# Kernel tuning notes

Hardware: AMD Instinct MI355X
Metric: run time of the kernel (lower is better)

Reference implementation:

```python
import jax, jax.numpy as jnp
import numpy as np

B, T, C, NH = 4, 827, 1024, 16
HS = C // NH
SCALE = 1.0 / float(np.sqrt(HS))


def setup_inputs() -> dict:
    key = jax.random.key(0)
    ks = jax.random.split(key, 16)
    d = {}
    d["x"] = jax.random.normal(ks[0], (B, T, C), jnp.float32)
    d["x_kv"] = jax.random.normal(ks[1], (B, T, C), jnp.float32)
    d["h"] = jax.random.normal(ks[2], (B, NH, T, T), jnp.float32) * 0.1
    for i, name in enumerate(["f01", "f02", "f12", "b01", "b02", "b12"]):
        d[name] = jax.random.uniform(ks[3 + i], (B, 256, 256), jnp.float32)
    for i, name in enumerate(["Wq", "Wk", "Wv", "Wp"]):
        d[name] = jax.random.normal(ks[9 + i], (C, C), jnp.float32) * 0.02
    for name in ["bq", "bk", "bv", "bp"]:
        d[name] = jnp.zeros((C,), jnp.float32)
    return d


def _sm(a):
    return jax.nn.softmax(a, axis=-1)


def reference(x, x_kv, h, f01, f02, f12, b01, b02, b12,
              Wq, bq, Wk, bk, Wv, bv, Wp, bp):
    Bb, Tt, Cc = x.shape

    def heads(t):  # [B,T,C] -> [B,NH,T,HS]
        return t.reshape(Bb, Tt, NH, HS).transpose(0, 2, 1, 3)

    q = heads(x @ Wq.T + bq)
    k = heads(x_kv @ Wk.T + bk)
    v = heads(x_kv @ Wv.T + bv)

    att = jnp.einsum('bhqd,bhkd->bhqk', q, k) * SCALE + h  # adaptive bias add

    # region-specific partial softmax (frame1->frame0, frame2->frame0, frame2->frame1)
    att = att.at[:, :, 285:541, 0:256].set(_sm(att[:, :, 285:541, 0:256]))
    att = att.at[:, :, 571:827, 0:256].set(_sm(att[:, :, 571:827, 0:256]))
    att = att.at[:, :, 571:827, 286:542].set(_sm(att[:, :, 571:827, 286:542]))

    # bidirectional epipolar maps (backward maps used transposed)
    b01t = b01.transpose(0, 2, 1)
    b02t = b02.transpose(0, 2, 1)
    b12t = b12.transpose(0, 2, 1)
    m12 = (f12 * b12t >= 0.1).astype(att.dtype)  # [B,256,256]

    # bi_epi_ratio (T==827 branch), computed BEFORE the multiplicative masking
    r3 = att[:, :, 571:827, 286:542]            # [B,NH,256,256]
    att_mean = r3.mean(-1)                       # [B,NH,256]
    att_mask_mean = (r3 * m12[:, None]).sum(-1) / m12.sum(-1)[:, None]
    bi_epi_ratio = att_mask_mean.mean(1) / att_mean.mean(1)  # [B,256]

    # att_for: forward-only masking (clone); att: forward*backward masking
    att_for = att
    att_for = att_for.at[:, :, 285:541, 0:256].multiply(f01[:, None])
    att_for = att_for.at[:, :, 571:827, 0:256].multiply(f02[:, None])
    att_for = att_for.at[:, :, 571:827, 286:542].multiply(f12[:, None])
    att = att.at[:, :, 285:541, 0:256].multiply((b01t * f01)[:, None])
    att = att.at[:, :, 571:827, 0:256].multiply((b02t * f02)[:, None])
    att = att.at[:, :, 571:827, 286:542].multiply((b12t * f12)[:, None])

    causal = jnp.tril(jnp.ones((Tt, Tt), dtype=bool))
    aw = jnp.where(causal, att, -jnp.inf)
    # re-softmax of the already masked+multiplied regions (overwrites, then global softmax)
    aw = aw.at[:, :, 571:827, 0:256].set(_sm(att[:, :, 571:827, 0:256]))
    aw = aw.at[:, :, 571:827, 286:542].set(_sm(att[:, :, 571:827, 286:542]))
    aw = _sm(aw)

    y = jnp.einsum('bhqk,bhkd->bhqd', aw, v)
    y = y.transpose(0, 2, 1, 3).reshape(Bb, Tt, Cc)
    y = y @ Wp.T + bp  # resid dropout is identity (pdrop=0 / eval)
    return y, bi_epi_ratio
```

## Files before the change

### kernel.cpp

```cpp
#include <hip/hip_runtime.h>
#include <cstdint>
#include <cstddef>

#define Tn  827
#define Cn  1024
#define BTn 3308
#define TPn 832
#define YSZ 3387392

typedef unsigned short u16;
typedef unsigned short u16x4 __attribute__((ext_vector_type(4)));
typedef __bf16 bf16_t;
typedef bf16_t bf16x8 __attribute__((ext_vector_type(8)));
typedef float f32x4 __attribute__((ext_vector_type(4)));

__device__ inline u16 f32_to_bf16(float f) {
  union { float f; unsigned u; } v; v.f = f;
  unsigned u = v.u;
  u += 0x7fffu + ((u >> 16) & 1u);
  return (u16)(u >> 16);
}

__global__ __launch_bounds__(256)
void cvt_all_k(const float* __restrict__ x, const float* __restrict__ xkv,
               const float* __restrict__ wq, const float* __restrict__ wk,
               const float* __restrict__ wv, const float* __restrict__ wp,
               u16* __restrict__ xb, u16* __restrict__ xkb,
               u16* __restrict__ wqb, u16* __restrict__ wkb,
               u16* __restrict__ wvb, u16* __restrict__ wpb,
               u16* __restrict__ Vt)
{
  const long NX = 846848;
  const long NW = 262144;
  long qidx = (long)blockIdx.x * 256 + threadIdx.x;
  const float* s; u16* d; long base;
  if (qidx < NX)            { s = x;   d = xb;  base = qidx; }
  else if (qidx < 2 * NX)   { s = xkv; d = xkb; base = qidx - NX; }
  else {
    long w = qidx - 2 * NX;
    int wi = (int)(w / NW);
    if (wi >= 4) {
      long p = w - 4 * NW;
      if (p < 20480) {
        int row = (int)(p / 5);
        int col = 827 + (int)(p - (long)row * 5);
        Vt[(size_t)row * TPn + col] = 0;
      }
      return;
    }
    base = w - (long)wi * NW;
    if      (wi == 0) { s = wq; d = wqb; }
    else if (wi == 1) { s = wk; d = wkb; }
    else if (wi == 2) { s = wv; d = wvb; }
    else              { s = wp; d = wpb; }
  }
  const float4 v = *(const float4*)(s + base * 4);
  u16x4 o;
  o.x = f32_to_bf16(v.x); o.y = f32_to_bf16(v.y);
  o.z = f32_to_bf16(v.z); o.w = f32_to_bf16(v.w);
  *(u16x4*)(d + base * 4) = o;
}

__global__ __launch_bounds__(256)
void gemm_qkv_k(const u16* __restrict__ xb, const u16* __restrict__ xkb,
                const u16* __restrict__ wqb, const u16* __restrict__ wkb,
                const u16* __restrict__ wvb,
                const float* __restrict__ bq, const float* __restrict__ bk,
                const float* __restrict__ bv,
                u16* __restrict__ Qb, u16* __restrict__ Kb, u16* __restrict__ Vt)
{
  const int zz = blockIdx.z;
  const u16* A  = (zz == 0) ? xb : xkb;
  const u16* Bw = (zz == 0) ? wqb : (zz == 1) ? wkb : wvb;
  const float* bias = (zz == 0) ? bq : (zz == 1) ? bk : bv;

  const int tid  = threadIdx.x;
  const int lane = tid & 63;
  const int wave = tid >> 6;
  const int wm = wave >> 1, wn = wave & 1;
  const int m0 = blockIdx.x * 128;
  const int n0 = blockIdx.y * 128;

  __shared__ u16 As[128 * 32];
  __shared__ u16 Bs[128 * 32];

  f32x4 acc[4][4];
  const f32x4 zero4 = {0.f, 0.f, 0.f, 0.f};
  #pragma unroll
  for (int i = 0; i < 4; ++i)
    #pragma unroll
    for (int j = 0; j < 4; ++j)
      acc[i][j] = zero4;

  for (int kt = 0; kt < 32; ++kt) {
    const int k0 = kt << 5;
    __syncthreads();
    #pragma unroll
    for (int it = 0; it < 2; ++it) {
      const int cbase = it * 256 + wave * 64;
      const int c  = cbase + lane;
      const int r  = c >> 2;
      const int ko = (c & 3) << 3;
      if (m0 + r < BTn)
        __builtin_amdgcn_global_load_lds(
            (__attribute__((address_space(1))) void*)(A + (size_t)(m0 + r) * Cn + k0 + ko),
            (__attribute__((address_space(3))) void*)(As + cbase * 8),
            16, 0, 0);
      __builtin_amdgcn_global_load_lds(
          (__attribute__((address_space(1))) void*)(Bw + (size_t)(n0 + r) * Cn + k0 + ko),
          (__attribute__((address_space(3))) void*)(Bs + cbase * 8),
          16, 0, 0);
    }
    __syncthreads();

    bf16x8 af[4], bfr[4];
    #pragma unroll
    for (int i = 0; i < 4; ++i) {
      const int r = wm * 64 + i * 16 + (lane & 15);
      af[i] = *(const bf16x8*)(As + r * 32 + ((lane >> 4) << 3));
    }
    #pragma unroll
    for (int j = 0; j < 4; ++j) {
      const int r = wn * 64 + j * 16 + (lane & 15);
      bfr[j] = *(const bf16x8*)(Bs + r * 32 + ((lane >> 4) << 3));
    }
    #pragma unroll
    for (int i = 0; i < 4; ++i)
      #pragma unroll
      for (int j = 0; j < 4; ++j)
        acc[i][j] = __builtin_amdgcn_mfma_f32_16x16x32_bf16(af[i], bfr[j], acc[i][j], 0, 0, 0);
  }

  const int cq = lane >> 4, cl = lane & 15;
  if (zz < 2) {
    u16* D = (zz == 0) ? Qb : Kb;
    #pragma unroll
    for (int i = 0; i < 4; ++i) {
      #pragma unroll
      for (int j = 0; j < 4; ++j) {
        const int rb  = m0 + wm * 64 + i * 16 + cq * 4;
        const int col = n0 + wn * 64 + j * 16 + cl;
        const float bc = bias[col];
        #pragma unroll
        for (int r = 0; r < 4; ++r) {
          const int row = rb + r;
          if (row < BTn) D[(size_t)row * Cn + col] = f32_to_bf16(acc[i][j][r] + bc);
        }
      }
    }
  } else {
    #pragma unroll
    for (int j = 0; j < 4; ++j) {
      const int col = n0 + wn * 64 + j * 16 + cl;
      const int hh = col >> 6, dd = col & 63;
      const float bc = bias[col];
      #pragma unroll
      for (int i = 0; i < 4; ++i) {
        const int rb = m0 + wm * 64 + i * 16 + cq * 4;
        #pragma unroll
        for (int r = 0; r < 4; ++r) {
          const int row = rb + r;
          if (row < BTn) {
            const int bb = row / Tn;
            const int t  = row - bb * Tn;
            Vt[((size_t)((bb * 16 + hh) * 64 + dd)) * TPn + t] = f32_to_bf16(acc[i][j][r] + bc);
          }
        }
      }
    }
  }
}

template<int BM, int BN, int MODE>
__global__ __launch_bounds__(256)
void gemm_k(const u16* __restrict__ Aall, const u16* __restrict__ Ball,
            const float* __restrict__ bias, float* __restrict__ Cf,
            u16* __restrict__ Cb, int M, int N, int K, int lda, int ldb, int ldc)
{
  static_assert(BM == 128, "BM fixed at 128");
  constexpr int TM = BM / 32;
  constexpr int TN = BN / 32;

  const int tid  = threadIdx.x;
  const int lane = tid & 63;
  const int wave = tid >> 6;
  const int wm = wave >> 1, wn = wave & 1;
  const int m0 = blockIdx.x * BM;
  const int n0 = blockIdx.y * BN;

  __shared__ u16 As[BM * 32];
  __shared__ u16 Bs[BN * 32];

  f32x4 acc[TM][TN];
  const f32x4 zero4 = {0.f, 0.f, 0.f, 0.f};
  #pragma unroll
  for (int i = 0; i < TM; ++i)
    #pragma unroll
    for (int j = 0; j < TN; ++j)
      acc[i][j] = zero4;

  const int nk = K >> 5;

  for (int kt = 0; kt < nk; ++kt) {
    const int k0 = kt << 5;
    __syncthreads();
    #pragma unroll
    for (int it = 0; it < BM / 64; ++it) {
      const int cbase = it * 256 + wave * 64;
      const int c  = cbase + lane;
      const int r  = c >> 2;
      const int ko = (c & 3) << 3;
      if (m0 + r < M)
        __builtin_amdgcn_global_load_lds(
            (__attribute__((address_space(1))) void*)(Aall + (size_t)(m0 + r) * lda + k0 + ko),
            (__attribute__((address_space(3))) void*)(As + cbase * 8),
            16, 0, 0);
    }
    #pragma unroll
    for (int it = 0; it < BN / 64; ++it) {
      const int cbase = it * 256 + wave * 64;
      const int c  = cbase + lane;
      const int r  = c >> 2;
      const int ko = (c & 3) << 3;
      if (n0 + r < N)
        __builtin_amdgcn_global_load_lds(
            (__attribute__((address_space(1))) void*)(Ball + (size_t)(n0 + r) * ldb + k0 + ko),
            (__attribute__((address_space(3))) void*)(Bs + cbase * 8),
            16, 0, 0);
    }
    __syncthreads();

    bf16x8 af[TM], bfr[TN];
    #pragma unroll
    for (int i = 0; i < TM; ++i) {
      const int r = wm * 64 + i * 16 + (lane & 15);
      af[i] = *(const bf16x8*)(As + r * 32 + ((lane >> 4) << 3));
    }
    #pragma unroll
    for (int j = 0; j < TN; ++j) {
      const int r = wn * (TN * 16) + j * 16 + (lane & 15);
      bfr[j] = *(const bf16x8*)(Bs + r * 32 + ((lane >> 4) << 3));
    }
    #pragma unroll
    for (int i = 0; i < TM; ++i)
      #pragma unroll
      for (int j = 0; j < TN; ++j)
        acc[i][j] = __builtin_amdgcn_mfma_f32_16x16x32_bf16(af[i], bfr[j], acc[i][j], 0, 0, 0);
  }

  const int cq = lane >> 4, cl = lane & 15;
  #pragma unroll
  for (int i = 0; i < TM; ++i) {
    #pragma unroll
    for (int j = 0; j < TN; ++j) {
      const int rb  = m0 + wm * 64 + i * 16 + cq * 4;
      const int col = n0 + wn * (TN * 16) + j * 16 + cl;
      #pragma unroll
      for (int r = 0; r < 4; ++r) {
        const int row = rb + r;
        const float v = acc[i][j][r];
        if constexpr (MODE == 0) {
          if (row < M) Cb[(size_t)row * ldc + col] = f32_to_bf16(v + bias[col]);
        } else {
          if (row < M) Cf[(size_t)row * ldc + col] = v + bias[col];
        }
      }
    }
  }
}

__global__ __launch_bounds__(256)
void btrans_k(const float* __restrict__ b01, const float* __restrict__ b02,
              const float* __restrict__ b12, float* __restrict__ bT)
{
  const int mb = blockIdx.z;
  const int rg = mb >> 2, bb = mb & 3;
  const float* src = (rg == 0 ? b01 : rg == 1 ? b02 : b12) + (size_t)bb * 65536;
  float* dst = bT + (size_t)mb * 65536;
  const int i0 = blockIdx.x * 64, j0 = blockIdx.y * 64;
  __shared__ float tile[64 * 65];
  const int tid = threadIdx.x;
  #pragma unroll
  for (int rep = 0; rep < 16; ++rep) {
    const int idx = rep * 256 + tid;
    const int jj = idx >> 6, ii = idx & 63;
    tile[ii * 65 + jj] = src[(size_t)(j0 + jj) * 256 + i0 + ii];
  }
  __syncthreads();
  #pragma unroll
  for (int rep = 0; rep < 16; ++rep) {
    const int idx = rep * 256 + tid;
    const int ii = idx >> 6, jj = idx & 63;
    dst[(size_t)(i0 + ii) * 256 + j0 + jj] = tile[ii * 65 + jj];
  }
}

__global__ __launch_bounds__(256)
void regfused_k(const u16* __restrict__ Qb, const u16* __restrict__ Kb,
                const float* __restrict__ hsrc,
                const float* __restrict__ f01, const float* __restrict__ f02,
                const float* __restrict__ f12, const float* __restrict__ bT,
                float* __restrict__ Sreg, float* __restrict__ mmOut,
                float* __restrict__ amOut)
{
  const int zr = blockIdx.y;
  const int rg = zr % 3;
  const int z  = zr / 3;
  const int b = z >> 4, hh = z & 15;
  const int qoff = (rg == 0) ? 285 : 571;
  const int koff = (rg == 2) ? 286 : 0;
  const int m0 = blockIdx.x * 64;

  const int tid = threadIdx.x, lane = tid & 63, wave = tid >> 6;
  const int quad = lane >> 4, cl = lane & 15;

  __shared__ u16 Qs[2 * 2048];
  __shared__ u16 Ks[2 * 8192];

  const u16* qsrc = Qb + ((size_t)(b * Tn + qoff + m0)) * Cn + hh * 64;
  const u16* ksrc = Kb + ((size_t)(b * Tn + koff)) * Cn + hh * 64;
  {
    const int r  = tid >> 2;
    const int ko = (tid & 3) << 3;
    #pragma unroll
    for (int p = 0; p < 2; ++p) {
      __builtin_amdgcn_global_load_lds(
          (__attribute__((address_space(1))) void*)(qsrc + (size_t)r * Cn + p * 32 + ko),
          (__attribute__((address_space(3))) void*)(&Qs[p * 2048 + wave * 512]), 16, 0, 0);
      #pragma unroll
      for (int it = 0; it < 4; ++it) {
        const int c  = it * 256 + tid;
        const int rr = c >> 2;
        const int kko = (c & 3) << 3;
        __builtin_amdgcn_global_load_lds(
            (__attribute__((address_space(1))) void*)(ksrc + (size_t)rr * Cn + p * 32 + kko),
            (__attribute__((address_space(3))) void*)(&Ks[p * 8192 + it * 2048 + wave * 512]), 16, 0, 0);
      }
    }
  }
  __syncthreads();

  bf16x8 qa[2];
  #pragma unroll
  for (int p = 0; p < 2; ++p)
    qa[p] = *(const bf16x8*)(&Qs[p * 2048 + (wave * 16 + cl) * 32 + quad * 8]);

  f32x4 acc[16];
  const f32x4 zero4 = {0.f, 0.f, 0.f, 0.f};
  #pragma unroll
  for (int n = 0; n < 16; ++n) acc[n] = zero4;

  #pragma unroll
  for (int p = 0; p < 2; ++p)
    #pragma unroll
    for (int n = 0; n < 16; ++n) {
      const bf16x8 kb = *(const bf16x8*)(&Ks[p * 8192 + (n * 16 + cl) * 32 + quad * 8]);
      acc[n] = __builtin_amdgcn_mfma_f32_16x16x32_bf16(qa[p], kb, acc[n], 0, 0, 0);
    }

  const int i0 = m0 + wave * 16 + quad * 4;
  const float* hp = hsrc + (size_t)z * Tn * Tn + (size_t)(qoff + i0) * Tn + koff + cl;
  #pragma unroll
  for (int nb = 0; nb < 4; ++nb) {
    float hv[4][4];
    #pragma unroll
    for (int n2 = 0; n2 < 4; ++n2)
      #pragma unroll
      for (int r = 0; r < 4; ++r)
        hv[n2][r] = hp[(size_t)r * Tn + (nb * 4 + n2) * 16];
    #pragma unroll
    for (int n2 = 0; n2 < 4; ++n2)
      #pragma unroll
      for (int r = 0; r < 4; ++r)
        acc[nb * 4 + n2][r] = acc[nb * 4 + n2][r] * 0.125f + hv[n2][r];
  }

  float red[4];
  #pragma unroll
  for (int r = 0; r < 4; ++r) {
    float m = acc[0][r];
    #pragma unroll
    for (int n = 1; n < 16; ++n) m = fmaxf(m, acc[n][r]);
    m = fmaxf(m, __shfl_xor(m, 1));
    m = fmaxf(m, __shfl_xor(m, 2));
    m = fmaxf(m, __shfl_xor(m, 4));
    m = fmaxf(m, __shfl_xor(m, 8));
    red[r] = m;
  }
  #pragma unroll
  for (int n = 0; n < 16; ++n)
    #pragma unroll
    for (int r = 0; r < 4; ++r)
      acc[n][r] = __expf(acc[n][r] - red[r]);
  #pragma unroll
  for (int r = 0; r < 4; ++r) {
    float s = 0.f;
    #pragma unroll
    for (int n = 0; n < 16; ++n) s += acc[n][r];
    s += __shfl_xor(s, 1); s += __shfl_xor(s, 2);
    s += __shfl_xor(s, 4); s += __shfl_xor(s, 8);
    const float inv = 1.f / s;
    #pragma unroll
    for (int n = 0; n < 16; ++n) acc[n][r] *= inv;
  }

  const float* fp  = (rg == 0) ? f01 : (rg == 1) ? f02 : f12;
  const float* fpb = fp + ((size_t)b * 256 + i0) * 256 + cl;
  const float* bpb = bT + (((size_t)(rg * 4 + b)) << 16) + (size_t)i0 * 256 + cl;
  float msum[4] = {0.f, 0.f, 0.f, 0.f};
  float mcnt[4] = {0.f, 0.f, 0.f, 0.f};
  float asum[4] = {0.f, 0.f, 0.f, 0.f};
  #pragma unroll
  for (int nb = 0; nb < 4; ++nb) {
    float fv[4][4], bv[4][4];
    #pragma unroll
    for (int n2 = 0; n2 < 4; ++n2)
      #pragma unroll
      for (int r = 0; r < 4; ++r) {
        fv[n2][r] = fpb[(size_t)r * 256 + (nb * 4 + n2) * 16];
        bv[n2][r] = bpb[(size_t)r * 256 + (nb * 4 + n2) * 16];
      }
    #pragma unroll
    for (int n2 = 0; n2 < 4; ++n2)
      #pragma unroll
      for (int r = 0; r < 4; ++r) {
        const int n = nb * 4 + n2;
        const float prod = fv[n2][r] * bv[n2][r];
        if (rg == 2) {
          const float mk = (prod >= 0.1f) ? 1.f : 0.f;
          msum[r] += acc[n][r] * mk;
          mcnt[r] += mk;
          asum[r] += acc[n][r];
        }
        acc[n][r] *= prod;
      }
  }
  if (rg == 2) {
    #pragma unroll
    for (int r = 0; r < 4; ++r) {
      msum[r] += __shfl_xor(msum[r], 1); msum[r] += __shfl_xor(msum[r], 2);
      msum[r] += __shfl_xor(msum[r], 4); msum[r] += __shfl_xor(msum[r], 8);
      mcnt[r] += __shfl_xor(mcnt[r], 1); mcnt[r] += __shfl_xor(mcnt[r], 2);
      mcnt[r] += __shfl_xor(mcnt[r], 4); mcnt[r] += __shfl_xor(mcnt[r], 8);
      asum[r] += __shfl_xor(asum[r], 1); asum[r] += __shfl_xor(asum[r], 2);
      asum[r] += __shfl_xor(asum[r], 4); asum[r] += __shfl_xor(asum[r], 8);
    }
    if (cl == 0) {
      #pragma unroll
      for (int r = 0; r < 4; ++r) {
        const int idx = ((b * 16 + hh) << 8) + i0 + r;
        mmOut[idx] = msum[r] / mcnt[r];
        amOut[idx] = asum[r] * (1.f / 256.f);
      }
    }
  }

  if (rg != 0) {
    #pragma unroll
    for (int r = 0; r < 4; ++r) {
      float m = acc[0][r];
      #pragma unroll
      for (int n = 1; n < 16; ++n) m = fmaxf(m, acc[n][r]);
      m = fmaxf(m, __shfl_xor(m, 1));
      m = fmaxf(m, __shfl_xor(m, 2));
      m = fmaxf(m, __shfl_xor(m, 4));
      m = fmaxf(m, __shfl_xor(m, 8));
      red[r] = m;
    }
    #pragma unroll
    for (int n = 0; n < 16; ++n)
      #pragma unroll
      for (int r = 0; r < 4; ++r)
        acc[n][r] = __expf(acc[n][r] - red[r]);
    #pragma unroll
    for (int r = 0; r < 4; ++r) {
      float s = 0.f;
      #pragma unroll
      for (int n = 0; n < 16; ++n) s += acc[n][r];
      s += __shfl_xor(s, 1); s += __shfl_xor(s, 2);
      s += __shfl_xor(s, 4); s += __shfl_xor(s, 8);
      const float inv = 1.f / s;
      #pragma unroll
      for (int n = 0; n < 16; ++n) acc[n][r] *= inv;
    }
  }
  float* outp = Sreg + (((size_t)zr) << 16) + (size_t)i0 * 256 + cl;
  #pragma unroll
  for (int n = 0; n < 16; ++n)
    #pragma unroll
    for (int r = 0; r < 4; ++r)
      outp[(size_t)r * 256 + n * 16] = acc[n][r];
}

__global__ __launch_bounds__(256)
void flash_k(const u16* __restrict__ Qb, const u16* __restrict__ Kb,
             const u16* __restrict__ Vt, const float* __restrict__ hsrc,
             const float* __restrict__ Sreg, u16* __restrict__ ya)
{
  const int bid = blockIdx.x;
  const int zlow = bid & 7;
  const int t = bid >> 3;
  const int qt = t % 13;
  const int zhigh = t / 13;
  const int z = zhigh * 8 + zlow;
  const int b = z >> 4, hh = z & 15;
  const int q0 = qt * 64;

  const int tid = threadIdx.x;
  const int lane = tid & 63;
  const int wave = tid >> 6;
  const int quad = lane >> 4;
  const int cl = lane & 15;

  __shared__ u16 Qs[2][2048];
  __shared__ u16 Ks[2][2048];
  __shared__ u16 Vs[2][2048];
  __shared__ u16 Ps[4][2][512];

  {
    const u16* src = Qb + ((size_t)(b * Tn + q0)) * Cn + hh * 64;
    const int r = tid >> 2;
    const int ko = (tid & 3) << 3;
    #pragma unroll
    for (int p = 0; p < 2; ++p)
      __builtin_amdgcn_global_load_lds(
          (__attribute__((address_space(1))) void*)(src + (size_t)r * Cn + p * 32 + ko),
          (__attribute__((address_space(3))) void*)(&Qs[p][wave * 512]), 16, 0, 0);
  }
  __syncthreads();

  bf16x8 qa[2];
  #pragma unroll
  for (int p = 0; p < 2; ++p)
    qa[p] = *(const bf16x8*)(&Qs[p][(wave * 16 + cl) * 32 + quad * 8]);

  f32x4 Oa[4];
  const f32x4 zero4 = {0.f, 0.f, 0.f, 0.f};
  Oa[0] = zero4; Oa[1] = zero4; Oa[2] = zero4; Oa[3] = zero4;
  float mrow[4] = {-3.0e38f, -3.0e38f, -3.0e38f, -3.0e38f};
  float lrow[4] = {0.f, 0.f, 0.f, 0.f};

  const size_t hbase = (size_t)z * Tn * Tn;
  const int qrow_base = q0 + wave * 16 + quad * 4;

  for (int kt = 0; kt <= qt; ++kt) {
    const int k0 = kt * 64;
    __syncthreads();
    {
      const u16* ksrc = Kb + ((size_t)(b * Tn + k0)) * Cn + hh * 64;
      const u16* vsrc = Vt + ((size_t)(z * 64)) * TPn + k0;
      const int r = tid >> 2;
      const int ko = (tid & 3) << 3;
      #pragma unroll
      for (int p = 0; p < 2; ++p) {
        __builtin_amdgcn_global_load_lds(
            (__attribute__((address_space(1))) void*)(ksrc + (size_t)r * Cn + p * 32 + ko),
            (__attribute__((address_space(3))) void*)(&Ks[p][wave * 512]), 16, 0, 0);
        __builtin_amdgcn_global_load_lds(
            (__attribute__((address_space(1))) void*)(vsrc + (size_t)r * TPn + p * 32 + ko),
            (__attribute__((address_space(3))) void*)(&Vs[p][wave * 512]), 16, 0, 0);
      }
    }
    float hv[4][4];
    unsigned rmask = 0;
    #pragma unroll
    for (int j = 0; j < 4; ++j) {
      const int kk = k0 + j * 16 + cl;
      #pragma unroll
      for (int r = 0; r < 4; ++r) {
        const int qq = qrow_base + r;
        const float* p = hsrc + hbase + (size_t)qq * Tn + kk;
        bool isreg = false;
        if (kk < 542) {
          if (qq >= 571 && qq < Tn) {
            if (kk < 256) {
              p = Sreg + (((size_t)(z * 3 + 1)) << 16) + (size_t)(qq - 571) * 256 + kk;
              isreg = true;
            } else if (kk >= 286) {
              p = Sreg + (((size_t)(z * 3 + 2)) << 16) + (size_t)(qq - 571) * 256 + (kk - 286);
              isreg = true;
            }
          } else if (qq >= 285 && qq < 541 && kk < 256) {
            p = Sreg + (((size_t)(z * 3 + 0)) << 16) + (size_t)(qq - 285) * 256 + kk;
            isreg = true;
          }
        }
        const bool valid = (kk <= qq) && (qq < Tn);
        hv[j][r] = valid ? *p : 0.f;
        if (isreg) rmask |= 1u << (j * 4 + r);
      }
    }
    __syncthreads();

    f32x4 sa[4];
    sa[0] = zero4; sa[1] = zero4; sa[2] = zero4; sa[3] = zero4;
    #pragma unroll
    for (int p = 0; p < 2; ++p) {
      #pragma unroll
      for (int n = 0; n < 4; ++n) {
        const bf16x8 kb = *(const bf16x8*)(&Ks[p][(n * 16 + cl) * 32 + quad * 8]);
        sa[n] = __builtin_amdgcn_mfma_f32_16x16x32_bf16(qa[p], kb, sa[n], 0, 0, 0);
      }
    }

    #pragma unroll
    for (int r = 0; r < 4; ++r) {
      const int qq = qrow_base + r;
      float sv[4];
      #pragma unroll
      for (int j = 0; j < 4; ++j) {
        const int kk = k0 + j * 16 + cl;
        const float vv = ((rmask >> (j * 4 + r)) & 1)
                             ? hv[j][r]
                             : sa[j][r] * 0.125f + hv[j][r];
        sv[j] = (kk <= qq && qq < Tn) ? vv : -3.0e38f;
      }
      float mx = fmaxf(fmaxf(sv[0], sv[1]), fmaxf(sv[2], sv[3]));
      mx = fmaxf(mx, __shfl_xor(mx, 1));
      mx = fmaxf(mx, __shfl_xor(mx, 2));
      mx = fmaxf(mx, __shfl_xor(mx, 4));
      mx = fmaxf(mx, __shfl_xor(mx, 8));
      const float mnew = fmaxf(mrow[r], mx);
      const float alpha = __expf(mrow[r] - mnew);
      mrow[r] = mnew;
      float ps[4], psum = 0.f;
      #pragma unroll
      for (int j = 0; j < 4; ++j) { ps[j] = __expf(sv[j] - mnew); psum += ps[j]; }
      psum += __shfl_xor(psum, 1);
      psum += __shfl_xor(psum, 2);
      psum += __shfl_xor(psum, 4);
      psum += __shfl_xor(psum, 8);
      lrow[r] = lrow[r] * alpha + psum;
      #pragma unroll
      for (int n = 0; n < 4; ++n) Oa[n][r] *= alpha;
      #pragma unroll
      for (int j = 0; j < 4; ++j)
        Ps[wave][j >> 1][(quad * 4 + r) * 32 + (j & 1) * 16 + cl] = f32_to_bf16(ps[j]);
    }

    #pragma unroll
    for (int p = 0; p < 2; ++p) {
      const bf16x8 pa = *(const bf16x8*)(&Ps[wave][p][cl * 32 + quad * 8]);
      #pragma unroll
      for (int n = 0; n < 4; ++n) {
        const bf16x8 vb = *(const bf16x8*)(&Vs[p][(n * 16 + cl) * 32 + quad * 8]);
        Oa[n] = __builtin_amdgcn_mfma_f32_16x16x32_bf16(pa, vb, Oa[n], 0, 0, 0);
      }
    }
  }

  #pragma unroll
  for (int r = 0; r < 4; ++r) {
    const int qq = qrow_base + r;
    if (qq >= Tn) continue;
    const float inv = 1.f / lrow[r];
    u16* op = ya + ((size_t)(b * Tn + qq)) * Cn + hh * 64;
    #pragma unroll
    for (int n = 0; n < 4; ++n)
      op[n * 16 + cl] = f32_to_bf16(Oa[n][r] * inv);
  }
}

__global__ __launch_bounds__(256)
void ratio_k(const float* __restrict__ mm, const float* __restrict__ am,
             float* __restrict__ out)
{
  const int idx = blockIdx.x * 256 + threadIdx.x;
  const int b = idx >> 8, i = idx & 255;
  float smm = 0.f, sam = 0.f;
  #pragma unroll
  for (int hh = 0; hh < 16; ++hh) {
    smm += mm[(b * 16 + hh) * 256 + i];
    sam += am[(b * 16 + hh) * 256 + i];
  }
  out[idx] = smm / sam;
}

extern "C" void kernel_launch(void* const* d_in, const int* in_sizes, int n_in,
                              void* d_out, int out_size, void* d_ws, size_t ws_size,
                              hipStream_t stream)
{
  (void)in_sizes; (void)n_in; (void)out_size;

  const float* x   = (const float*)d_in[0];
  const float* xkv = (const float*)d_in[1];
  const float* hb  = (const float*)d_in[2];
  const float* f01 = (const float*)d_in[3];
  const float* f02 = (const float*)d_in[4];
  const float* f12 = (const float*)d_in[5];
  const float* b01 = (const float*)d_in[6];
  const float* b02 = (const float*)d_in[7];
  const float* b12 = (const float*)d_in[8];
  const float* Wq  = (const float*)d_in[9];
  const float* Wk  = (const float*)d_in[10];
  const float* Wv  = (const float*)d_in[11];
  const float* Wp  = (const float*)d_in[12];
  const float* bq  = (const float*)d_in[13];
  const float* bk  = (const float*)d_in[14];
  const float* bv  = (const float*)d_in[15];
  const float* bp  = (const float*)d_in[16];
  float* out = (float*)d_out;

  char* ws = (char*)d_ws;
  u16* xb   = (u16*)(ws + 0);
  u16* xkb  = (u16*)(ws + 6774784);
  u16* wqb  = (u16*)(ws + 13549568);
  u16* wkb  = (u16*)(ws + 15646720);
  u16* wvb  = (u16*)(ws + 17743872);
  u16* wpb  = (u16*)(ws + 19841024);
  u16* Qb   = (u16*)(ws + 21938176);
  u16* Kb   = (u16*)(ws + 28712960);
  u16* Vt   = (u16*)(ws + 42262528);
  u16* ya   = (u16*)(ws + 49078272);
  float* Sreg = (float*)(ws + 55853056);
  float* bT = (float*)(ws + 106184704);
  float* mm = (float*)(ws + 109330432);
  float* am = (float*)(ws + 109395968);
  const size_t need = 109461504;
  if (ws_size < need) return;

  cvt_all_k<<<dim3(10792), 256, 0, stream>>>(x, xkv, Wq, Wk, Wv, Wp,
                                             xb, xkb, wqb, wkb, wvb, wpb, Vt);
  btrans_k<<<dim3(4, 4, 12), 256, 0, stream>>>(b01, b02, b12, bT);
  gemm_qkv_k<<<dim3(26, 8, 3), 256, 0, stream>>>(xb, xkb, wqb, wkb, wvb,
                                                 bq, bk, bv, Qb, Kb, Vt);
  regfused_k<<<dim3(4, 192), 256, 0, stream>>>(Qb, Kb, hb, f01, f02, f12, bT,
                                               Sreg, mm, am);
  ratio_k<<<dim3(4), 256, 0, stream>>>(mm, am, out + YSZ);
  flash_k<<<dim3(832), 256, 0, stream>>>(Qb, Kb, Vt, hb, Sreg, ya);
  gemm_k<128, 64, 3><<<dim3(26, 16, 1), 256, 0, stream>>>(ya, wpb, bp, out, nullptr,
                                                          BTn, Cn, Cn, Cn, Cn, Cn);
}
```

Measured before the change: 421.0 us.

## Double-buffer LDS tiles in GEMMs and prefetch K/V plus bias in attention

The QKV and output GEMMs now use two LDS buffers, so the next k-tile's global_load_lds is issued before the MFMAs on the current tile, leaving one barrier per iteration. The flash-attention kernel likewise double-buffers its K/V tiles and loads the next tile's bias/region values into registers one iteration ahead, using precomputed per-row pointers and applying the causal mask only on the diagonal tile. The aim is to hide global-memory latency behind compute. In exchange it doubles LDS use and adds registers in the attention kernel, which may lower occupancy.

```diff
diff --git a/kernel.cpp b/kernel.cpp
--- a/kernel.cpp
+++ b/kernel.cpp
@@ -13,6 +13,10 @@
 typedef __bf16 bf16_t;
 typedef bf16_t bf16x8 __attribute__((ext_vector_type(8)));
 typedef float f32x4 __attribute__((ext_vector_type(4)));
+
+#define GLD(gp, lp) __builtin_amdgcn_global_load_lds( \
+    (__attribute__((address_space(1))) void*)(gp),    \
+    (__attribute__((address_space(3))) void*)(lp), 16, 0, 0)
 
 __device__ inline u16 f32_to_bf16(float f) {
   union { float f; unsigned u; } v; v.f = f;
@@ -81,8 +85,8 @@
   const int m0 = blockIdx.x * 128;
   const int n0 = blockIdx.y * 128;
 
-  __shared__ u16 As[128 * 32];
-  __shared__ u16 Bs[128 * 32];
+  __shared__ u16 As[2][4096];
+  __shared__ u16 Bs[2][4096];
 
   f32x4 acc[4][4];
   const f32x4 zero4 = {0.f, 0.f, 0.f, 0.f};
@@ -92,44 +96,46 @@
     for (int j = 0; j < 4; ++j)
       acc[i][j] = zero4;
 
+#define QKV_STAGE(buf_, kt_) do {                                        \
+    const int k0_ = (kt_) << 5;                                          \
+    _Pragma("unroll")                                                    \
+    for (int it = 0; it < 2; ++it) {                                     \
+      const int cbase = it * 256 + wave * 64;                            \
+      const int c  = cbase + lane;                                       \
+      const int r_ = c >> 2;                                             \
+      const int ko_ = (c & 3) << 3;                                      \
+      if (m0 + r_ < BTn)                                                 \
+        GLD(A  + (size_t)(m0 + r_) * Cn + k0_ + ko_, As[buf_] + cbase * 8); \
+      GLD(Bw + (size_t)(n0 + r_) * Cn + k0_ + ko_, Bs[buf_] + cbase * 8);  \
+    }                                                                    \
+  } while (0)
+
+  QKV_STAGE(0, 0);
+  __syncthreads();
+
   for (int kt = 0; kt < 32; ++kt) {
-    const int k0 = kt << 5;
-    __syncthreads();
-    #pragma unroll
-    for (int it = 0; it < 2; ++it) {
-      const int cbase = it * 256 + wave * 64;
-      const int c  = cbase + lane;
-      const int r  = c >> 2;
-      const int ko = (c & 3) << 3;
-      if (m0 + r < BTn)
-        __builtin_amdgcn_global_load_lds(
-            (__attribute__((address_space(1))) void*)(A + (size_t)(m0 + r) * Cn + k0 + ko),
-            (__attribute__((address_space(3))) void*)(As + cbase * 8),
-            16, 0, 0);
-      __builtin_amdgcn_global_load_lds(
-          (__attribute__((address_space(1))) void*)(Bw + (size_t)(n0 + r) * Cn + k0 + ko),
-          (__attribute__((address_space(3))) void*)(Bs + cbase * 8),
-          16, 0, 0);
-    }
-    __syncthreads();
+    const int cur = kt & 1;
+    if (kt < 31) QKV_STAGE(cur ^ 1, kt + 1);
 
     bf16x8 af[4], bfr[4];
     #pragma unroll
     for (int i = 0; i < 4; ++i) {
       const int r = wm * 64 + i * 16 + (lane & 15);
-      af[i] = *(const bf16x8*)(As + r * 32 + ((lane >> 4) << 3));
+      af[i] = *(const bf16x8*)(As[cur] + r * 32 + ((lane >> 4) << 3));
     }
     #pragma unroll
     for (int j = 0; j < 4; ++j) {
       const int r = wn * 64 + j * 16 + (lane & 15);
-      bfr[j] = *(const bf16x8*)(Bs + r * 32 + ((lane >> 4) << 3));
+      bfr[j] = *(const bf16x8*)(Bs[cur] + r * 32 + ((lane >> 4) << 3));
     }
     #pragma unroll
     for (int i = 0; i < 4; ++i)
       #pragma unroll
       for (int j = 0; j < 4; ++j)
         acc[i][j] = __builtin_amdgcn_mfma_f32_16x16x32_bf16(af[i], bfr[j], acc[i][j], 0, 0, 0);
-  }
+    __syncthreads();
+  }
+#undef QKV_STAGE
 
   const int cq = lane >> 4, cl = lane & 15;
   if (zz < 2) {
@@ -188,8 +194,8 @@
   const int m0 = blockIdx.x * BM;
   const int n0 = blockIdx.y * BN;
 
-  __shared__ u16 As[BM * 32];
-  __shared__ u16 Bs[BN * 32];
+  __shared__ u16 As[2][BM * 32];
+  __shared__ u16 Bs[2][BN * 32];
 
   f32x4 acc[TM][TN];
   const f32x4 zero4 = {0.f, 0.f, 0.f, 0.f};
@@ -201,52 +207,54 @@
 
   const int nk = K >> 5;
 
+#define OUT_STAGE(buf_, kt_) do {                                         \
+    const int k0_ = (kt_) << 5;                                           \
+    _Pragma("unroll")                                                     \
+    for (int it = 0; it < BM / 64; ++it) {                                \
+      const int cbase = it * 256 + wave * 64;                             \
+      const int c  = cbase + lane;                                        \
+      const int r_ = c >> 2;                                              \
+      const int ko_ = (c & 3) << 3;                                       \
+      if (m0 + r_ < M)                                                    \
+        GLD(Aall + (size_t)(m0 + r_) * lda + k0_ + ko_, As[buf_] + cbase * 8); \
+    }                                                                     \
+    _Pragma("unroll")                                                     \
+    for (int it = 0; it < BN / 64; ++it) {                                \
+      const int cbase = it * 256 + wave * 64;                             \
+      const int c  = cbase + lane;                                        \
+      const int r_ = c >> 2;                                              \
+      const int ko_ = (c & 3) << 3;                                       \
+      if (n0 + r_ < N)                                                    \
+        GLD(Ball + (size_t)(n0 + r_) * ldb + k0_ + ko_, Bs[buf_] + cbase * 8); \
+    }                                                                     \
+  } while (0)
+
+  OUT_STAGE(0, 0);
+  __syncthreads();
+
   for (int kt = 0; kt < nk; ++kt) {
-    const int k0 = kt << 5;
-    __syncthreads();
-    #pragma unroll
-    for (int it = 0; it < BM / 64; ++it) {
-      const int cbase = it * 256 + wave * 64;
-      const int c  = cbase + lane;
-      const int r  = c >> 2;
-      const int ko = (c & 3) << 3;
-      if (m0 + r < M)
-        __builtin_amdgcn_global_load_lds(
-            (__attribute__((address_space(1))) void*)(Aall + (size_t)(m0 + r) * lda + k0 + ko),
-            (__attribute__((address_space(3))) void*)(As + cbase * 8),
-            16, 0, 0);
-    }
-    #pragma unroll
-    for (int it = 0; it < BN / 64; ++it) {
-      const int cbase = it * 256 + wave * 64;
-      const int c  = cbase + lane;
-      const int r  = c >> 2;
-      const int ko = (c & 3) << 3;
-      if (n0 + r < N)
-        __builtin_amdgcn_global_load_lds(
-            (__attribute__((address_space(1))) void*)(Ball + (size_t)(n0 + r) * ldb + k0 + ko),
-            (__attribute__((address_space(3))) void*)(Bs + cbase * 8),
-            16, 0, 0);
-    }
-    __syncthreads();
+    const int cur = kt & 1;
+    if (kt + 1 < nk) OUT_STAGE(cur ^ 1, kt + 1);
 
     bf16x8 af[TM], bfr[TN];
     #pragma unroll
     for (int i = 0; i < TM; ++i) {
       const int r = wm * 64 + i * 16 + (lane & 15);
-      af[i] = *(const bf16x8*)(As + r * 32 + ((lane >> 4) << 3));
+      af[i] = *(const bf16x8*)(As[cur] + r * 32 + ((lane >> 4) << 3));
     }
     #pragma unroll
     for (int j = 0; j < TN; ++j) {
       const int r = wn * (TN * 16) + j * 16 + (lane & 15);
-      bfr[j] = *(const bf16x8*)(Bs + r * 32 + ((lane >> 4) << 3));
+      bfr[j] = *(const bf16x8*)(Bs[cur] + r * 32 + ((lane >> 4) << 3));
     }
     #pragma unroll
     for (int i = 0; i < TM; ++i)
       #pragma unroll
       for (int j = 0; j < TN; ++j)
         acc[i][j] = __builtin_amdgcn_mfma_f32_16x16x32_bf16(af[i], bfr[j], acc[i][j], 0, 0, 0);
-  }
+    __syncthreads();
+  }
+#undef OUT_STAGE
 
   const int cq = lane >> 4, cl = lane & 15;
   #pragma unroll
@@ -324,17 +332,14 @@
     const int ko = (tid & 3) << 3;
     #pragma unroll
     for (int p = 0; p < 2; ++p) {
-      __builtin_amdgcn_global_load_lds(
-          (__attribute__((address_space(1))) void*)(qsrc + (size_t)r * Cn + p * 32 + ko),
-          (__attribute__((address_space(3))) void*)(&Qs[p * 2048 + wave * 512]), 16, 0, 0);
+      GLD(qsrc + (size_t)r * Cn + p * 32 + ko, &Qs[p * 2048 + wave * 512]);
       #pragma unroll
       for (int it = 0; it < 4; ++it) {
         const int c  = it * 256 + tid;
         const int rr = c >> 2;
         const int kko = (c & 3) << 3;
-        __builtin_amdgcn_global_load_lds(
-            (__attribute__((address_space(1))) void*)(ksrc + (size_t)rr * Cn + p * 32 + kko),
-            (__attribute__((address_space(3))) void*)(&Ks[p * 8192 + it * 2048 + wave * 512]), 16, 0, 0);
+        GLD(ksrc + (size_t)rr * Cn + p * 32 + kko,
+            &Ks[p * 8192 + it * 2048 + wave * 512]);
       }
     }
   }
@@ -513,8 +518,8 @@
   const int cl = lane & 15;
 
   __shared__ u16 Qs[2][2048];
-  __shared__ u16 Ks[2][2048];
-  __shared__ u16 Vs[2][2048];
+  __shared__ u16 Ks[2][2][2048];
+  __shared__ u16 Vs[2][2][2048];
   __shared__ u16 Ps[4][2][512];
 
   {
@@ -523,10 +528,83 @@
     const int ko = (tid & 3) << 3;
     #pragma unroll
     for (int p = 0; p < 2; ++p)
-      __builtin_amdgcn_global_load_lds(
-          (__attribute__((address_space(1))) void*)(src + (size_t)r * Cn + p * 32 + ko),
-          (__attribute__((address_space(3))) void*)(&Qs[p][wave * 512]), 16, 0, 0);
-  }
+      GLD(src + (size_t)r * Cn + p * 32 + ko, &Qs[p][wave * 512]);
+  }
+
+  const u16* ksrc0 = Kb + ((size_t)(b * Tn)) * Cn + hh * 64;
+  const u16* vsrc0 = Vt + ((size_t)(z * 64)) * TPn;
+  const int sr  = tid >> 2;
+  const int sko = (tid & 3) << 3;
+
+#define STAGE_KV(buf_, k0_) do {                                          \
+    const u16* ks_ = ksrc0 + (size_t)((k0_) + sr) * Cn;                   \
+    const u16* vs_ = vsrc0 + (size_t)sr * TPn + (k0_);                    \
+    _Pragma("unroll")                                                     \
+    for (int p = 0; p < 2; ++p) {                                         \
+      GLD(ks_ + p * 32 + sko, &Ks[buf_][p][wave * 512]);                  \
+      GLD(vs_ + p * 32 + sko, &Vs[buf_][p][wave * 512]);                  \
+    }                                                                     \
+  } while (0)
+
+  const int qrow_base = q0 + wave * 16 + quad * 4;
+  const size_t hbase = (size_t)z * Tn * Tn;
+  const float* hrow[4];
+  const float* preg1[4];
+  const float* preg2[4];
+  int cat[4];
+  #pragma unroll
+  for (int r = 0; r < 4; ++r) {
+    const int qq = qrow_base + r;
+    const int qc = (qq < Tn) ? qq : (Tn - 1);
+    hrow[r] = hsrc + hbase + (size_t)qc * Tn;
+    if (qq >= 571 && qq < Tn) {
+      cat[r] = 2;
+      preg1[r] = Sreg + (((size_t)(z * 3 + 1)) << 16) + (size_t)(qq - 571) * 256;
+      preg2[r] = Sreg + (((size_t)(z * 3 + 2)) << 16) + (size_t)(qq - 571) * 256 - 286;
+    } else if (qq >= 285 && qq < 541) {
+      cat[r] = 1;
+      preg1[r] = Sreg + (((size_t)(z * 3 + 0)) << 16) + (size_t)(qq - 285) * 256;
+      preg2[r] = hrow[r];
+    } else {
+      cat[r] = 0;
+      preg1[r] = hrow[r];
+      preg2[r] = hrow[r];
+    }
+  }
+
+#define GATHER(hv_, rm_, k0_) do {                                        \
+    rm_ = 0;                                                              \
+    if ((k0_) < 542) {                                                    \
+      _Pragma("unroll")                                                   \
+      for (int j = 0; j < 4; ++j) {                                       \
+        const int kk = (k0_) + j * 16 + cl;                               \
+        _Pragma("unroll")                                                 \
+        for (int r = 0; r < 4; ++r) {                                     \
+          const float* p = hrow[r] + kk;                                  \
+          bool isr = false;                                               \
+          if (cat[r] == 2) {                                              \
+            if (kk < 256)       { p = preg1[r] + kk; isr = true; }        \
+            else if (kk >= 286 && kk < 542) { p = preg2[r] + kk; isr = true; } \
+          } else if (cat[r] == 1) {                                       \
+            if (kk < 256)       { p = preg1[r] + kk; isr = true; }        \
+          }                                                               \
+          hv_[j * 4 + r] = *p;                                            \
+          if (isr) rm_ |= 1u << (j * 4 + r);                              \
+        }                                                                 \
+      }                                                                   \
+    } else {                                                              \
+      _Pragma("unroll")                                                   \
+      for (int j = 0; j < 4; ++j) {                                       \
+        const int kk = (k0_) + j * 16 + cl;                               \
+        _Pragma("unroll")                                                 \
+        for (int r = 0; r < 4; ++r) hv_[j * 4 + r] = hrow[r][kk];         \
+      }                                                                   \
+    }                                                                     \
+  } while (0)
+
+  STAGE_KV(0, 0);
+  float hv_cur[16]; unsigned rmask_cur;
+  GATHER(hv_cur, rmask_cur, 0);
   __syncthreads();
 
   bf16x8 qa[2];
@@ -540,57 +618,16 @@
   float mrow[4] = {-3.0e38f, -3.0e38f, -3.0e38f, -3.0e38f};
   float lrow[4] = {0.f, 0.f, 0.f, 0.f};
 
-  const size_t hbase = (size_t)z * Tn * Tn;
-  const int qrow_base = q0 + wave * 16 + quad * 4;
-
   for (int kt = 0; kt <= qt; ++kt) {
+    const int cur = kt & 1;
     const int k0 = kt * 64;
-    __syncthreads();
-    {
-      const u16* ksrc = Kb + ((size_t)(b * Tn + k0)) * Cn + hh * 64;
-      const u16* vsrc = Vt + ((size_t)(z * 64)) * TPn + k0;
-      const int r = tid >> 2;
-      const int ko = (tid & 3) << 3;
-      #pragma unroll
-      for (int p = 0; p < 2; ++p) {
-        __builtin_amdgcn_global_load_lds(
-            (__attribute__((address_space(1))) void*)(ksrc + (size_t)r * Cn + p * 32 + ko),
-            (__attribute__((address_space(3))) void*)(&Ks[p][wave * 512]), 16, 0, 0);
-        __builtin_amdgcn_global_load_lds(
-            (__attribute__((address_space(1))) void*)(vsrc + (size_t)r * TPn + p * 32 + ko),
-            (__attribute__((address_space(3))) void*)(&Vs[p][wave * 512]), 16, 0, 0);
-      }
-    }
-    float hv[4][4];
-    unsigned rmask = 0;
-    #pragma unroll
-    for (int j = 0; j < 4; ++j) {
-      const int kk = k0 + j * 16 + cl;
-      #pragma unroll
-      for (int r = 0; r < 4; ++r) {
-        const int qq = qrow_base + r;
-        const float* p = hsrc + hbase + (size_t)qq * Tn + kk;
-        bool isreg = false;
-        if (kk < 542) {
-          if (qq >= 571 && qq < Tn) {
-            if (kk < 256) {
-              p = Sreg + (((size_t)(z * 3 + 1)) << 16) + (size_t)(qq - 571) * 256 + kk;
-              isreg = true;
-            } else if (kk >= 286) {
-              p = Sreg + (((size_t)(z * 3 + 2)) << 16) + (size_t)(qq - 571) * 256 + (kk - 286);
-              isreg = true;
-            }
-          } else if (qq >= 285 && qq < 541 && kk < 256) {
-            p = Sreg + (((size_t)(z * 3 + 0)) << 16) + (size_t)(qq - 285) * 256 + kk;
-            isreg = true;
-          }
-        }
-        const bool valid = (kk <= qq) && (qq < Tn);
-        hv[j][r] = valid ? *p : 0.f;
-        if (isreg) rmask |= 1u << (j * 4 + r);
-      }
-    }
-    __syncthreads();
+    const bool diag = (kt == qt);
+
+    float hv_nxt[16]; unsigned rmask_nxt = 0;
+    if (kt < qt) {
+      STAGE_KV(cur ^ 1, k0 + 64);
+      GATHER(hv_nxt, rmask_nxt, k0 + 64);
+    }
 
     f32x4 sa[4];
     sa[0] = zero4; sa[1] = zero4; sa[2] = zero4; sa[3] = zero4;
@@ -598,7 +635,7 @@
     for (int p = 0; p < 2; ++p) {
       #pragma unroll
       for (int n = 0; n < 4; ++n) {
-        const bf16x8 kb = *(const bf16x8*)(&Ks[p][(n * 16 + cl) * 32 + quad * 8]);
+        const bf16x8 kb = *(const bf16x8*)(&Ks[cur][p][(n * 16 + cl) * 32 + quad * 8]);
         sa[n] = __builtin_amdgcn_mfma_f32_16x16x32_bf16(qa[p], kb, sa[n], 0, 0, 0);
       }
     }
@@ -610,10 +647,10 @@
       #pragma unroll
       for (int j = 0; j < 4; ++j) {
         const int kk = k0 + j * 16 + cl;
-        const float vv = ((rmask >> (j * 4 + r)) & 1)
-                             ? hv[j][r]
-                             : sa[j][r] * 0.125f + hv[j][r];
-        sv[j] = (kk <= qq && qq < Tn) ? vv : -3.0e38f;
+        const float vv = ((rmask_cur >> (j * 4 + r)) & 1)
+                             ? hv_cur[j * 4 + r]
+                             : sa[j][r] * 0.125f + hv_cur[j * 4 + r];
+        sv[j] = (diag && !(kk <= qq && qq < Tn)) ? -3.0e38f : vv;
       }
       float mx = fmaxf(fmaxf(sv[0], sv[1]), fmaxf(sv[2], sv[3]));
       mx = fmaxf(mx, __shfl_xor(mx, 1));
@@ -643,11 +680,21 @@
       const bf16x8 pa = *(const bf16x8*)(&Ps[wave][p][cl * 32 + quad * 8]);
       #pragma unroll
       for (int n = 0; n < 4; ++n) {
-        const bf16x8 vb = *(const bf16x8*)(&Vs[p][(n * 16 + cl) * 32 + quad * 8]);
+        const bf16x8 vb = *(const bf16x8*)(&Vs[cur][p][(n * 16 + cl) * 32 + quad * 8]);
         Oa[n] = __builtin_amdgcn_mfma_f32_16x16x32_bf16(pa, vb, Oa[n], 0, 0, 0);
       }
     }
-  }
+
+    __syncthreads();
+
+    if (kt < qt) {
+      #pragma unroll
+      for (int i2 = 0; i2 < 16; ++i2) hv_cur[i2] = hv_nxt[i2];
+      rmask_cur = rmask_nxt;
+    }
+  }
+#undef STAGE_KV
+#undef GATHER
 
   #pragma unroll
   for (int r = 0; r < 4; ++r) {
```

Result: slower. 490.4 us (+16.5%).
